# Optimization experiments

Measured on AMD Instinct MI355X. Metric: run time of the kernel, lower is better.

Reference implementation:

```python
import jax, jax.numpy as jnp
import numpy as np

NP_, NA_ = 50000, 20000
D_IN, D_HID, D_OUT = 128, 128, 64
E_W, E_C, E_R = 250000, 500000, 250000


def setup_inputs() -> dict:
    key = jax.random.key(0)
    ks = jax.random.split(key, 14)
    s_in = 1.0 / np.sqrt(D_IN)
    s_h = 1.0 / np.sqrt(D_HID)
    return {
        "x_paper": jax.random.normal(ks[0], (NP_, D_IN), jnp.float32),
        "x_author": jax.random.normal(ks[1], (NA_, D_IN), jnp.float32),
        "Wl1": jax.random.normal(ks[2], (3, D_HID, D_IN), jnp.float32) * s_in,
        "bl1": jax.random.normal(ks[3], (3, D_HID), jnp.float32) * 0.01,
        "Wr1": jax.random.normal(ks[4], (3, D_HID, D_IN), jnp.float32) * s_in,
        "Wl2": jax.random.normal(ks[5], (3, D_OUT, D_HID), jnp.float32) * s_h,
        "bl2": jax.random.normal(ks[6], (3, D_OUT), jnp.float32) * 0.01,
        "Wr2": jax.random.normal(ks[7], (3, D_OUT, D_HID), jnp.float32) * s_h,
        "writes_src": jax.random.randint(ks[8], (E_W,), 0, NA_),
        "writes_dst": jax.random.randint(ks[9], (E_W,), 0, NP_),
        "cites_src": jax.random.randint(ks[10], (E_C,), 0, NP_),
        "cites_dst": jax.random.randint(ks[11], (E_C,), 0, NP_),
        "rev_src": jax.random.randint(ks[12], (E_R,), 0, NP_),
        "rev_dst": jax.random.randint(ks[13], (E_R,), 0, NA_),
    }


def _sage(x_src, x_dst, src, dst, Wl, bl, Wr, n_dst):
    # PyG SAGEConv(aggr='mean'): lin_l(mean_j x_src[j]) + lin_r(x_dst)
    agg = jax.ops.segment_sum(x_src[src], dst, num_segments=n_dst)
    cnt = jax.ops.segment_sum(jnp.ones_like(dst, dtype=x_src.dtype), dst,
                              num_segments=n_dst)
    agg = agg / jnp.maximum(cnt, 1.0)[:, None]  # degree-0 nodes -> 0 (PyG scatter-mean)
    return agg @ Wl.T + bl + x_dst @ Wr.T


def reference(x_paper, x_author, Wl1, bl1, Wr1, Wl2, bl2, Wr2,
              writes_src, writes_dst, cites_src, cites_dst, rev_src, rev_dst):
    def hetero_layer(xp, xa, Wl, bl, Wr):
        # HeteroConv(aggr='mean'): average per-relation outputs per dst node type
        op = 0.5 * (_sage(xa, xp, writes_src, writes_dst, Wl[0], bl[0], Wr[0], NP_)
                    + _sage(xp, xp, cites_src, cites_dst, Wl[1], bl[1], Wr[1], NP_))
        oa = _sage(xp, xa, rev_src, rev_dst, Wl[2], bl[2], Wr[2], NA_)
        return op, oa

    hp, ha = hetero_layer(x_paper, x_author, Wl1, bl1, Wr1)
    hp, ha = jax.nn.relu(hp), jax.nn.relu(ha)  # norm_type='none', dropout eval-mode
    hp, _ = hetero_layer(hp, ha, Wl2, bl2, Wr2)
    return hp  # logits for category='paper', [NP_, D_OUT]
```

## Files before the change

### kernel.cpp

```cpp
#include <hip/hip_runtime.h>

#define NP 50000
#define NA 20000
#define E_W 250000
#define E_C 500000
#define E_R 250000
#define E_TOT (E_W + E_C + E_R)
#define CAP 48
#define RBLK 4096
#define NSEG 245
#define NCHP 782
#define NCHA 313
#define NBIN (NCHP + NCHA)

typedef __attribute__((ext_vector_type(8))) short short8;
typedef __attribute__((ext_vector_type(4))) float floatx4;
typedef __attribute__((ext_vector_type(2))) float floatx2;

__device__ __forceinline__ unsigned short f2bf(float f) {
    unsigned u = __float_as_uint(f);
    return (unsigned short)((u + 0x7FFFu + ((u >> 16) & 1u)) >> 16);
}
__device__ __forceinline__ float bflo(unsigned v) { return __uint_as_float(v << 16); }
__device__ __forceinline__ float bfhi(unsigned v) { return __uint_as_float(v & 0xFFFF0000u); }

__device__ __forceinline__ int frag_off(int NT, int j, int n, int k) {
    int t = n >> 4, ln = n & 15;
    int kb = k >> 5, q = (k >> 3) & 3, r = k & 7;
    return (((j * NT + t) * 4 + kb) * 64 + q * 16 + ln) * 8 + r;
}

__device__ __forceinline__ void prep_body(
    int idx,
    const float* __restrict__ xp, const float* __restrict__ xa,
    const float* __restrict__ Wl1, const float* __restrict__ Wr1,
    const float* __restrict__ Wl2, const float* __restrict__ Wr2,
    const float* __restrict__ bl1, const float* __restrict__ bl2,
    unsigned short* __restrict__ xpb, unsigned short* __restrict__ xab,
    unsigned* __restrict__ xp8, unsigned* __restrict__ xa8,
    unsigned short* __restrict__ Wp1, unsigned short* __restrict__ Wa1,
    unsigned short* __restrict__ Wt2, unsigned short* __restrict__ Wr2s,
    float* __restrict__ bias_p1, float* __restrict__ bias_a1,
    float* __restrict__ bias_p2) {
    const int n4p = NP * 32, n4a = NA * 32;
    if (idx < n4p + n4a) {
        const float* s; unsigned short* d; unsigned* d8; int i = idx;
        if (i < n4p) { s = xp; d = xpb; d8 = xp8; }
        else { s = xa; d = xab; d8 = xa8; i -= n4p; }
        float4 v = ((const float4*)s)[i];
        ushort4 u;
        u.x = f2bf(v.x); u.y = f2bf(v.y); u.z = f2bf(v.z); u.w = f2bf(v.w);
        ((ushort4*)d)[i] = u;
        int w = __builtin_amdgcn_cvt_pk_fp8_f32(v.x, v.y, 0, false);
        w = __builtin_amdgcn_cvt_pk_fp8_f32(v.z, v.w, w, true);
        d8[i] = (unsigned)w;
        return;
    }
    int j = idx - (n4p + n4a);
    if (j < 49152) {
        int jj = j >> 14, rem = j & 16383, n = rem >> 7, k = rem & 127;
        float v = (jj == 0)   ? 0.5f * Wl1[rem]
                  : (jj == 1) ? 0.5f * Wl1[16384 + rem]
                              : 0.5f * (Wr1[rem] + Wr1[16384 + rem]);
        Wp1[frag_off(8, jj, n, k)] = f2bf(v);
    } else if (j < 81920) {
        int i2 = j - 49152;
        int jj = i2 >> 14, rem = i2 & 16383, n = rem >> 7, k = rem & 127;
        float v = (jj == 0) ? Wl1[2 * 16384 + rem] : Wr1[2 * 16384 + rem];
        Wa1[frag_off(8, jj, n, k)] = f2bf(v);
    } else if (j < 98304) {
        int i2 = j - 81920;
        int jj = i2 >> 13, rem = i2 & 8191, n = rem >> 7, k = rem & 127;
        float v = 0.5f * Wl2[jj * 8192 + rem];
        Wt2[frag_off(4, jj, n, k)] = f2bf(v);
    } else if (j < 106496) {
        int i2 = j - 98304;
        int n = i2 >> 7, k = i2 & 127;
        float v = 0.5f * (Wr2[i2] + Wr2[8192 + i2]);
        Wr2s[frag_off(4, 0, n, k)] = f2bf(v);
    } else if (j < 106496 + 320) {
        int b = j - 106496;
        if (b < 128) bias_p1[b] = 0.5f * (bl1[b] + bl1[128 + b]);
        else if (b < 256) bias_a1[b - 128] = bl1[256 + b - 128];
        else bias_p2[b - 256] = 0.5f * (bl2[b - 256] + bl2[64 + b - 256]);
    }
}

__device__ __forceinline__ void edge_bin(
    int e, const int* __restrict__ w_src, const int* __restrict__ w_dst,
    const int* __restrict__ c_src, const int* __restrict__ c_dst,
    const int* __restrict__ r_src, const int* __restrict__ r_dst,
    int& bin, int& sub, int& src) {
    bool isC = (e >= E_W) & (e < E_W + E_C);
    bool isR = e >= E_W + E_C;
    const int* db = isR ? r_dst : (isC ? c_dst : w_dst);
    const int* sb = isR ? r_src : (isC ? c_src : w_src);
    int idx = e - (isC ? E_W : 0) - (isR ? (E_W + E_C) : 0);
    int d = db[idx];
    src = sb[idx];
    if (isR) { bin = NCHP + (d >> 6); sub = d & 63; }
    else { bin = d >> 6; sub = (d & 63) + (isC ? 64 : 0); }
}

__device__ __forceinline__ void route_body(
    int bid, const int* __restrict__ w_src, const int* __restrict__ w_dst,
    const int* __restrict__ c_src, const int* __restrict__ c_dst,
    const int* __restrict__ r_src, const int* __restrict__ r_dst,
    unsigned* __restrict__ seg, int* __restrict__ segoff, int* __restrict__ segcnt,
    int* cnt_s, int* base_s, int* cur_s) {
    int tid = threadIdx.x, lane = tid & 63;
    for (int k = tid; k < NBIN; k += 256) cnt_s[k] = 0;
    __syncthreads();
#pragma unroll 4
    for (int u = 0; u < 16; ++u) {
        int e = bid * RBLK + u * 256 + tid;
        if (e < E_TOT) {
            int bin, sub, src;
            edge_bin(e, w_src, w_dst, c_src, c_dst, r_src, r_dst, bin, sub, src);
            atomicAdd(&cnt_s[bin], 1);
        }
    }
    __syncthreads();
    if (tid < 64) {
        int v[18], tot = 0;
#pragma unroll
        for (int q = 0; q < 18; ++q) {
            int k = tid * 18 + q;
            v[q] = (k < NBIN) ? cnt_s[k] : 0;
            tot += v[q];
        }
        int sc = tot;
#pragma unroll
        for (int ofs = 1; ofs < 64; ofs <<= 1) {
            int t = __shfl_up(sc, ofs, 64);
            if (lane >= ofs) sc += t;
        }
        int run = sc - tot;
#pragma unroll
        for (int q = 0; q < 18; ++q) {
            int k = tid * 18 + q;
            if (k < NBIN) { base_s[k] = run; run += v[q]; }
        }
    }
    __syncthreads();
    for (int k = tid; k < NBIN; k += 256) {
        segoff[bid * NBIN + k] = base_s[k];
        segcnt[bid * NBIN + k] = cnt_s[k];
        cur_s[k] = base_s[k];
    }
    __syncthreads();
    unsigned* segb = seg + (size_t)bid * RBLK;
#pragma unroll 4
    for (int u = 0; u < 16; ++u) {
        int e = bid * RBLK + u * 256 + tid;
        if (e < E_TOT) {
            int bin, sub, src;
            edge_bin(e, w_src, w_dst, c_src, c_dst, r_src, r_dst, bin, sub, src);
            int pos = atomicAdd(&cur_s[bin], 1);
            segb[pos] = (unsigned)src | ((unsigned)sub << 16);
        }
    }
}

__global__ __launch_bounds__(256) void route_prep(
    const float* xp, const float* xa, const float* Wl1, const float* Wr1,
    const float* Wl2, const float* Wr2, const float* bl1, const float* bl2,
    unsigned short* xpb, unsigned short* xab, unsigned* xp8, unsigned* xa8,
    unsigned short* Wp1, unsigned short* Wa1, unsigned short* Wt2, unsigned short* Wr2s,
    float* bias_p1, float* bias_a1, float* bias_p2,
    const int* w_src, const int* w_dst, const int* c_src, const int* c_dst,
    const int* r_src, const int* r_dst,
    unsigned* seg, int* segoff, int* segcnt) {
    __shared__ int cnt_s[NBIN], base_s[NBIN], cur_s[NBIN];
    if ((int)blockIdx.x < NSEG)
        route_body(blockIdx.x, w_src, w_dst, c_src, c_dst, r_src, r_dst,
                   seg, segoff, segcnt, cnt_s, base_s, cur_s);
    else
        prep_body((blockIdx.x - NSEG) * 256 + threadIdx.x, xp, xa, Wl1, Wr1, Wl2, Wr2,
                  bl1, bl2, xpb, xab, xp8, xa8, Wp1, Wa1, Wt2, Wr2s,
                  bias_p1, bias_a1, bias_p2);
}

__global__ __launch_bounds__(512) void fill_l1(
    const unsigned* __restrict__ seg, const int* __restrict__ segoff,
    const int* __restrict__ segcnt, int* __restrict__ cnt,
    unsigned short* __restrict__ csr,
    const unsigned* __restrict__ xp8, const unsigned* __restrict__ xa8,
    const unsigned short* __restrict__ xpb, const unsigned short* __restrict__ xab,
    const unsigned short* __restrict__ Wp1, const float* __restrict__ bias_p1,
    const unsigned short* __restrict__ Wa1, const float* __restrict__ bias_a1,
    const unsigned short* __restrict__ Wt2, const unsigned short* __restrict__ Wr2s,
    unsigned short* __restrict__ ta, unsigned short* __restrict__ tp,
    float* __restrict__ sp) {
    __shared__ unsigned short rows[128 * CAP];
    __shared__ int cursor[128];
    __shared__ int offs[NSEG], cnts[NSEG];
    __shared__ __align__(16) unsigned short aggL[64][136];
    int tid = threadIdx.x;
    int k = blockIdx.x;
    bool isPaper = k < NCHP;
    int base = isPaper ? k * 64 : (k - NCHP) * 64;
    int total = isPaper ? NP : NA;
    int M = total - base; if (M > 64) M = 64;

    for (int s = tid; s < NSEG; s += 512) {
        offs[s] = segoff[s * NBIN + k];
        cnts[s] = segcnt[s * NBIN + k];
    }
    if (tid < 128) cursor[tid] = 0;
    __syncthreads();
    {
        int grp = tid >> 4, gl = tid & 15;
        for (int s = grp; s < NSEG; s += 32) {
            int n = cnts[s];
            const unsigned* spq = seg + (size_t)s * RBLK + offs[s];
            for (int i = gl; i < n; i += 16) {
                unsigned v = spq[i];
                int sub = v >> 16, srcn = v & 0xFFFFu;
                int pos = atomicAdd(&cursor[sub], 1);
                if (pos < CAP) rows[sub * CAP + pos] = (unsigned short)srcn;
            }
        }
    }
    __syncthreads();
    if (isPaper) {
        for (int r = tid; r < 2 * M; r += 512)
            cnt[base * 2 + r] = cursor[(r >> 1) + ((r & 1) << 6)];
        const unsigned* rU = (const unsigned*)rows;
        unsigned* cU = (unsigned*)csr + (size_t)base * 2 * (CAP / 2);
        for (int i = tid; i < 2 * M * (CAP / 2); i += 512) {
            int r = i / (CAP / 2), j = i - r * (CAP / 2);
            cU[i] = rU[((r >> 1) + ((r & 1) << 6)) * (CAP / 2) + j];
        }
    }

    int wave = tid >> 6, lane = tid & 63, ln = lane & 15, quad = lane >> 4;
    int wrow = (wave & 3) * 16, nhalf = wave >> 2;
    floatx4 acc[4];
#pragma unroll
    for (int t = 0; t < 4; ++t) acc[t] = (floatx4){0.f, 0.f, 0.f, 0.f};

    auto gather = [&](int rel, const unsigned* __restrict__ src8, int dummy) {
        int g = tid >> 5, sl = tid & 31;
        for (int l = g; l < 64; l += 16) {
            int deg = cursor[l + (rel << 6)];
            int degc = deg < CAP ? deg : CAP;
            const unsigned short* rp = &rows[(l + (rel << 6)) * CAP];
            float a0 = 0.f, a1 = 0.f, a2 = 0.f, a3 = 0.f;
            float b0 = 0.f, b1 = 0.f, b2 = 0.f, b3 = 0.f;
            for (int i = 0; i < degc; i += 8) {
                short8 rr = *(const short8*)&rp[i];
                unsigned v[8];
#pragma unroll
                for (int u = 0; u < 8; ++u) {
                    int ii = i + u;
                    int q = (ii < degc) ? (int)(unsigned short)rr[u] : dummy;
                    v[u] = src8[(q << 5) + sl];
                }
#pragma unroll
                for (int u = 0; u < 8; ++u) {
                    floatx2 lo = __builtin_amdgcn_cvt_pk_f32_fp8(v[u], false);
                    floatx2 hi = __builtin_amdgcn_cvt_pk_f32_fp8(v[u], true);
                    if (u & 1) { b0 += lo.x; b1 += lo.y; b2 += hi.x; b3 += hi.y; }
                    else       { a0 += lo.x; a1 += lo.y; a2 += hi.x; a3 += hi.y; }
                }
            }
            float scl = deg > 0 ? 1.f / (float)deg : 0.f;
            float r0 = (a0 + b0) * scl, r1 = (a1 + b1) * scl;
            float r2 = (a2 + b2) * scl, r3 = (a3 + b3) * scl;
            unsigned wlo = ((unsigned)f2bf(r1) << 16) | (unsigned)f2bf(r0);
            unsigned whi = ((unsigned)f2bf(r3) << 16) | (unsigned)f2bf(r2);
            *(uint2*)&aggL[l][sl * 4] = make_uint2(wlo, whi);
        }
    };
    auto gemm_lds = [&](const unsigned short* __restrict__ Wb) {
#pragma unroll
        for (int kb = 0; kb < 4; ++kb) {
            short8 af = *(const short8*)&aggL[wrow + ln][quad * 8 + kb * 32];
#pragma unroll
            for (int t = 0; t < 4; ++t) {
                short8 bf = *(const short8*)(Wb + ((nhalf * 4 + t) * 4 + kb) * 512 + lane * 8);
                acc[t] = __builtin_amdgcn_mfma_f32_16x16x32_bf16(af, bf, acc[t], 0, 0, 0);
            }
        }
    };
    auto gemm_glob = [&](const unsigned short* __restrict__ X,
                         const unsigned short* __restrict__ Wb) {
        int row = base + wrow + ln;
        int rowc = row < total ? row : total - 1;
        const unsigned short* A = X + (size_t)rowc * 128 + quad * 8;
#pragma unroll
        for (int kb = 0; kb < 4; ++kb) {
            short8 af = *(const short8*)(A + kb * 32);
#pragma unroll
            for (int t = 0; t < 4; ++t) {
                short8 bf = *(const short8*)(Wb + ((nhalf * 4 + t) * 4 + kb) * 512 + lane * 8);
                acc[t] = __builtin_amdgcn_mfma_f32_16x16x32_bf16(af, bf, acc[t], 0, 0, 0);
            }
        }
    };

    if (isPaper) {
        gather(0, xa8, NA);
        __syncthreads();
        gemm_lds(Wp1);
        __syncthreads();
        gather(1, xp8, NP);
        __syncthreads();
        gemm_lds(Wp1 + 16384);
        gemm_glob(xpb, Wp1 + 2 * 16384);
        __syncthreads();
    } else {
        gather(0, xp8, NP);
        __syncthreads();
        gemm_lds(Wa1);
        gemm_glob(xab, Wa1 + 16384);
        __syncthreads();
    }
    {
        const float* bias = isPaper ? bias_p1 : bias_a1;
#pragma unroll
        for (int t = 0; t < 4; ++t) {
            int col = nhalf * 64 + t * 16 + ln;
            float bv = bias[col];
#pragma unroll
            for (int r = 0; r < 4; ++r)
                aggL[wrow + quad * 4 + r][col] = f2bf(fmaxf(acc[t][r] + bv, 0.f));
        }
    }
    __syncthreads();
    floatx4 tacc[4];
#pragma unroll
    for (int t = 0; t < 4; ++t) tacc[t] = (floatx4){0.f, 0.f, 0.f, 0.f};
    int rows16 = (wave & 3) * 16;
    if (isPaper) {
        const unsigned short* W = (wave < 4) ? (Wt2 + 64 * 128) : Wr2s;
#pragma unroll
        for (int kb = 0; kb < 4; ++kb) {
            short8 af = *(const short8*)&aggL[rows16 + ln][quad * 8 + kb * 32];
#pragma unroll
            for (int t = 0; t < 4; ++t) {
                short8 bf = *(const short8*)(W + (t * 4 + kb) * 512 + lane * 8);
                tacc[t] = __builtin_amdgcn_mfma_f32_16x16x32_bf16(af, bf, tacc[t], 0, 0, 0);
            }
        }
#pragma unroll
        for (int t = 0; t < 4; ++t) {
            int col = t * 16 + ln;
#pragma unroll
            for (int r = 0; r < 4; ++r) {
                int lr = rows16 + quad * 4 + r;
                if (lr < M) {
                    if (wave < 4) tp[(size_t)(base + lr) * 64 + col] = f2bf(tacc[t][r]);
                    else sp[(size_t)(base + lr) * 64 + col] = tacc[t][r];
                }
            }
        }
    } else {
        int thalf = wave >> 2;
#pragma unroll
        for (int kb = 0; kb < 4; ++kb) {
            short8 af = *(const short8*)&aggL[rows16 + ln][quad * 8 + kb * 32];
#pragma unroll
            for (int tt = 0; tt < 2; ++tt) {
                short8 bf = *(const short8*)(Wt2 + ((thalf * 2 + tt) * 4 + kb) * 512 + lane * 8);
                tacc[tt] = __builtin_amdgcn_mfma_f32_16x16x32_bf16(af, bf, tacc[tt], 0, 0, 0);
            }
        }
#pragma unroll
        for (int tt = 0; tt < 2; ++tt) {
            int col = (thalf * 2 + tt) * 16 + ln;
#pragma unroll
            for (int r = 0; r < 4; ++r) {
                int lr = rows16 + quad * 4 + r;
                if (lr < M) ta[(size_t)(base + lr) * 64 + col] = f2bf(tacc[tt][r]);
            }
        }
    }
}

__global__ void agg2(const unsigned short* __restrict__ ta, const unsigned short* __restrict__ tp,
                     const int* __restrict__ cnt, const unsigned short* __restrict__ csr,
                     const float* __restrict__ sp_in, const float* __restrict__ bias_p2,
                     float* __restrict__ out) {
    int node = blockIdx.x * 8 + (threadIdx.x >> 5);
    if (node >= NP) return;
    int lane = threadIdx.x & 63;
    int sl = lane & 31;
    int hw = lane & 32;
    float r0 = 0.f, r1 = 0.f;
#pragma unroll
    for (int rel = 0; rel < 2; ++rel) {
        int dummy = (rel == 0) ? NA : NP;
        const unsigned* sp = (const unsigned*)((rel == 0) ? ta : tp);
        int idx = node * 2 + rel;
        int deg = cnt[idx];
        int degc = deg < CAP ? deg : CAP;
        const unsigned short* row = csr + (size_t)idx * CAP;
        int ei0 = (sl < degc) ? (int)row[sl] : dummy;
        int ei1 = (32 + sl < degc) ? (int)row[32 + sl] : dummy;
        int degw = degc;
        int other = __shfl_xor(degw, 32, 64);
        if (other > degw) degw = other;
        float s0 = 0.f, s1 = 0.f, t0 = 0.f, t1 = 0.f;
        for (int i = 0; i < degw; i += 8) {
            unsigned v[8];
#pragma unroll
            for (int u = 0; u < 8; ++u) {
                int ii = i + u;
                int esrc = (ii < 32) ? ei0 : ei1;
                int qq = __shfl(esrc, hw | (ii & 31), 64);
                qq = (ii < degc) ? qq : dummy;
                v[u] = sp[(qq << 5) + sl];
            }
#pragma unroll
            for (int u = 0; u < 8; ++u) {
                if (u & 1) { t0 += bflo(v[u]); t1 += bfhi(v[u]); }
                else       { s0 += bflo(v[u]); s1 += bfhi(v[u]); }
            }
        }
        float scl = deg > 0 ? 1.f / (float)deg : 0.f;
        r0 += (s0 + t0) * scl; r1 += (s1 + t1) * scl;
    }
    float2 spv = ((const float2*)sp_in)[(size_t)node * 32 + sl];
    float2 bv = ((const float2*)bias_p2)[sl];
    ((float2*)out)[(size_t)node * 32 + sl] =
        make_float2(r0 + spv.x + bv.x, r1 + spv.y + bv.y);
}

extern "C" void kernel_launch(void* const* d_in, const int* in_sizes, int n_in,
                              void* d_out, int out_size, void* d_ws, size_t ws_size,
                              hipStream_t stream) {
    (void)in_sizes; (void)n_in; (void)out_size; (void)ws_size;
    const float* xp  = (const float*)d_in[0];
    const float* xa  = (const float*)d_in[1];
    const float* Wl1 = (const float*)d_in[2];
    const float* bl1 = (const float*)d_in[3];
    const float* Wr1 = (const float*)d_in[4];
    const float* Wl2 = (const float*)d_in[5];
    const float* bl2 = (const float*)d_in[6];
    const float* Wr2 = (const float*)d_in[7];
    const int* w_src = (const int*)d_in[8];
    const int* w_dst = (const int*)d_in[9];
    const int* c_src = (const int*)d_in[10];
    const int* c_dst = (const int*)d_in[11];
    const int* r_src = (const int*)d_in[12];
    const int* r_dst = (const int*)d_in[13];
    float* out = (float*)d_out;

    char* p = (char*)d_ws;
    auto alloc = [&](size_t bytes) {
        char* r = p;
        p += (bytes + 255) & ~(size_t)255;
        return r;
    };
    unsigned short* xpb   = (unsigned short*)alloc((size_t)NP * 128 * 2);
    unsigned short* xab   = (unsigned short*)alloc((size_t)NA * 128 * 2);
    unsigned*       xp8   = (unsigned*)alloc((size_t)(NP + 1) * 128);
    unsigned*       xa8   = (unsigned*)alloc((size_t)(NA + 1) * 128);
    unsigned short* ta    = (unsigned short*)alloc((size_t)(NA + 1) * 64 * 2);
    unsigned short* tp    = (unsigned short*)alloc((size_t)(NP + 1) * 64 * 2);
    float*          sp    = (float*)alloc((size_t)NP * 64 * 4);
    int*            cnt    = (int*)alloc((size_t)NP * 2 * 4);
    unsigned short* csr    = (unsigned short*)alloc((size_t)NP * 2 * CAP * 2);
    unsigned*       seg    = (unsigned*)alloc((size_t)NSEG * RBLK * 4);
    int*            segoff = (int*)alloc((size_t)NSEG * NBIN * 4);
    int*            segcnt = (int*)alloc((size_t)NSEG * NBIN * 4);
    unsigned short* Wp1  = (unsigned short*)alloc(3 * 128 * 128 * 2);
    unsigned short* Wa1  = (unsigned short*)alloc(2 * 128 * 128 * 2);
    unsigned short* Wt2  = (unsigned short*)alloc(2 * 64 * 128 * 2);
    unsigned short* Wr2s = (unsigned short*)alloc(64 * 128 * 2);
    float* bias_p1 = (float*)alloc(128 * 4);
    float* bias_a1 = (float*)alloc(128 * 4);
    float* bias_p2 = (float*)alloc(64 * 4);

    hipMemsetAsync(xp8 + (size_t)NP * 32, 0, 128, stream);
    hipMemsetAsync(xa8 + (size_t)NA * 32, 0, 128, stream);
    hipMemsetAsync(ta + (size_t)NA * 64, 0, 128, stream);
    hipMemsetAsync(tp + (size_t)NP * 64, 0, 128, stream);

    int prep_threads = (NP + NA) * 32 + 106496 + 320;
    int prep_blocks = (prep_threads + 255) / 256;
    route_prep<<<NSEG + prep_blocks, 256, 0, stream>>>(
        xp, xa, Wl1, Wr1, Wl2, Wr2, bl1, bl2,
        xpb, xab, xp8, xa8, Wp1, Wa1, Wt2, Wr2s, bias_p1, bias_a1, bias_p2,
        w_src, w_dst, c_src, c_dst, r_src, r_dst, seg, segoff, segcnt);

    fill_l1<<<NBIN, 512, 0, stream>>>(seg, segoff, segcnt, cnt, csr,
                                      xp8, xa8, xpb, xab, Wp1, bias_p1, Wa1, bias_a1,
                                      Wt2, Wr2s, ta, tp, sp);

    agg2<<<(NP + 7) / 8, 256, 0, stream>>>(ta, tp, cnt, csr, sp, bias_p2, out);
}
```

Measured before the change: 199.1 us.

## Merge layer-1 relation gathers into one pass and halve routing segments

Routing blocks now cover 8192 edges each, halving the number of segments, and each segment's offset and count are packed into one 32-bit word. The layer-1 fused kernel gathers both relations (writes and cites) for all 128 local rows in a single pass, with each thread group processing two rows at once to get more loads in flight. The aggregation buffer is doubled to 128 rows so both GEMMs run back to back with fewer barriers, and the CSR write-out moves after the compute. The cost is more shared memory per block, which may reduce occupancy, and per-segment counts and offsets must stay below 65536.

```diff
diff --git a/kernel.cpp b/kernel.cpp
--- a/kernel.cpp
+++ b/kernel.cpp
@@ -7,8 +7,8 @@
 #define E_R 250000
 #define E_TOT (E_W + E_C + E_R)
 #define CAP 48
-#define RBLK 4096
-#define NSEG 245
+#define RBLK 8192
+#define NSEG 123
 #define NCHP 782
 #define NCHA 313
 #define NBIN (NCHP + NCHA)
@@ -106,13 +106,13 @@
     int bid, const int* __restrict__ w_src, const int* __restrict__ w_dst,
     const int* __restrict__ c_src, const int* __restrict__ c_dst,
     const int* __restrict__ r_src, const int* __restrict__ r_dst,
-    unsigned* __restrict__ seg, int* __restrict__ segoff, int* __restrict__ segcnt,
+    unsigned* __restrict__ seg, unsigned* __restrict__ segmeta,
     int* cnt_s, int* base_s, int* cur_s) {
     int tid = threadIdx.x, lane = tid & 63;
     for (int k = tid; k < NBIN; k += 256) cnt_s[k] = 0;
     __syncthreads();
 #pragma unroll 4
-    for (int u = 0; u < 16; ++u) {
+    for (int u = 0; u < 32; ++u) {
         int e = bid * RBLK + u * 256 + tid;
         if (e < E_TOT) {
             int bin, sub, src;
@@ -144,14 +144,13 @@
     }
     __syncthreads();
     for (int k = tid; k < NBIN; k += 256) {
-        segoff[bid * NBIN + k] = base_s[k];
-        segcnt[bid * NBIN + k] = cnt_s[k];
+        segmeta[bid * NBIN + k] = ((unsigned)base_s[k] << 16) | (unsigned)cnt_s[k];
         cur_s[k] = base_s[k];
     }
     __syncthreads();
     unsigned* segb = seg + (size_t)bid * RBLK;
 #pragma unroll 4
-    for (int u = 0; u < 16; ++u) {
+    for (int u = 0; u < 32; ++u) {
         int e = bid * RBLK + u * 256 + tid;
         if (e < E_TOT) {
             int bin, sub, src;
@@ -170,11 +169,11 @@
     float* bias_p1, float* bias_a1, float* bias_p2,
     const int* w_src, const int* w_dst, const int* c_src, const int* c_dst,
     const int* r_src, const int* r_dst,
-    unsigned* seg, int* segoff, int* segcnt) {
+    unsigned* seg, unsigned* segmeta) {
     __shared__ int cnt_s[NBIN], base_s[NBIN], cur_s[NBIN];
     if ((int)blockIdx.x < NSEG)
         route_body(blockIdx.x, w_src, w_dst, c_src, c_dst, r_src, r_dst,
-                   seg, segoff, segcnt, cnt_s, base_s, cur_s);
+                   seg, segmeta, cnt_s, base_s, cur_s);
     else
         prep_body((blockIdx.x - NSEG) * 256 + threadIdx.x, xp, xa, Wl1, Wr1, Wl2, Wr2,
                   bl1, bl2, xpb, xab, xp8, xa8, Wp1, Wa1, Wt2, Wr2s,
@@ -182,9 +181,8 @@
 }
 
 __global__ __launch_bounds__(512) void fill_l1(
-    const unsigned* __restrict__ seg, const int* __restrict__ segoff,
-    const int* __restrict__ segcnt, int* __restrict__ cnt,
-    unsigned short* __restrict__ csr,
+    const unsigned* __restrict__ seg, const unsigned* __restrict__ segmeta,
+    int* __restrict__ cnt, unsigned short* __restrict__ csr,
     const unsigned* __restrict__ xp8, const unsigned* __restrict__ xa8,
     const unsigned short* __restrict__ xpb, const unsigned short* __restrict__ xab,
     const unsigned short* __restrict__ Wp1, const float* __restrict__ bias_p1,
@@ -194,8 +192,8 @@
     float* __restrict__ sp) {
     __shared__ unsigned short rows[128 * CAP];
     __shared__ int cursor[128];
-    __shared__ int offs[NSEG], cnts[NSEG];
-    __shared__ __align__(16) unsigned short aggL[64][136];
+    __shared__ unsigned pkd[NSEG];
+    __shared__ __align__(16) unsigned short aggL[128][136];
     int tid = threadIdx.x;
     int k = blockIdx.x;
     bool isPaper = k < NCHP;
@@ -203,17 +201,15 @@
     int total = isPaper ? NP : NA;
     int M = total - base; if (M > 64) M = 64;
 
-    for (int s = tid; s < NSEG; s += 512) {
-        offs[s] = segoff[s * NBIN + k];
-        cnts[s] = segcnt[s * NBIN + k];
-    }
+    for (int s = tid; s < NSEG; s += 512) pkd[s] = segmeta[s * NBIN + k];
     if (tid < 128) cursor[tid] = 0;
     __syncthreads();
     {
         int grp = tid >> 4, gl = tid & 15;
         for (int s = grp; s < NSEG; s += 32) {
-            int n = cnts[s];
-            const unsigned* spq = seg + (size_t)s * RBLK + offs[s];
+            unsigned pk = pkd[s];
+            int n = pk & 0xFFFFu;
+            const unsigned* spq = seg + (size_t)s * RBLK + (pk >> 16);
             for (int i = gl; i < n; i += 16) {
                 unsigned v = spq[i];
                 int sub = v >> 16, srcn = v & 0xFFFFu;
@@ -223,6 +219,163 @@
         }
     }
     __syncthreads();
+    {
+        const unsigned* s0 = isPaper ? xa8 : xp8;
+        const unsigned* s1 = xp8;
+        int d0 = isPaper ? NA : NP, d1 = NP;
+        int LROWS = isPaper ? 128 : 64;
+        int g = tid >> 5, sl = tid & 31;
+        for (int l0 = g; l0 < LROWS; l0 += 32) {
+            int lA = l0, lB = l0 + 16;
+            const unsigned* sA = (lA & 64) ? s1 : s0;
+            const unsigned* sB = (lB & 64) ? s1 : s0;
+            int duA = (lA & 64) ? d1 : d0;
+            int duB = (lB & 64) ? d1 : d0;
+            int dA = cursor[lA], dB = cursor[lB];
+            int cA = dA < CAP ? dA : CAP, cB = dB < CAP ? dB : CAP;
+            int cm = cA > cB ? cA : cB;
+            const unsigned short* rpA = &rows[lA * CAP];
+            const unsigned short* rpB = &rows[lB * CAP];
+            float a0 = 0.f, a1 = 0.f, a2 = 0.f, a3 = 0.f;
+            float b0 = 0.f, b1 = 0.f, b2 = 0.f, b3 = 0.f;
+            for (int i = 0; i < cm; i += 8) {
+                short8 rA = *(const short8*)&rpA[i];
+                short8 rB = *(const short8*)&rpB[i];
+                unsigned vA[8], vB[8];
+#pragma unroll
+                for (int u = 0; u < 8; ++u) {
+                    int q = (i + u < cA) ? (int)(unsigned short)rA[u] : duA;
+                    vA[u] = sA[(q << 5) + sl];
+                }
+#pragma unroll
+                for (int u = 0; u < 8; ++u) {
+                    int q = (i + u < cB) ? (int)(unsigned short)rB[u] : duB;
+                    vB[u] = sB[(q << 5) + sl];
+                }
+#pragma unroll
+                for (int u = 0; u < 8; ++u) {
+                    floatx2 lo = __builtin_amdgcn_cvt_pk_f32_fp8(vA[u], false);
+                    floatx2 hi = __builtin_amdgcn_cvt_pk_f32_fp8(vA[u], true);
+                    a0 += lo.x; a1 += lo.y; a2 += hi.x; a3 += hi.y;
+                }
+#pragma unroll
+                for (int u = 0; u < 8; ++u) {
+                    floatx2 lo = __builtin_amdgcn_cvt_pk_f32_fp8(vB[u], false);
+                    floatx2 hi = __builtin_amdgcn_cvt_pk_f32_fp8(vB[u], true);
+                    b0 += lo.x; b1 += lo.y; b2 += hi.x; b3 += hi.y;
+                }
+            }
+            float sclA = dA > 0 ? 1.f / (float)dA : 0.f;
+            float sclB = dB > 0 ? 1.f / (float)dB : 0.f;
+            unsigned wloA = ((unsigned)f2bf(a1 * sclA) << 16) | (unsigned)f2bf(a0 * sclA);
+            unsigned whiA = ((unsigned)f2bf(a3 * sclA) << 16) | (unsigned)f2bf(a2 * sclA);
+            unsigned wloB = ((unsigned)f2bf(b1 * sclB) << 16) | (unsigned)f2bf(b0 * sclB);
+            unsigned whiB = ((unsigned)f2bf(b3 * sclB) << 16) | (unsigned)f2bf(b2 * sclB);
+            *(uint2*)&aggL[lA][sl * 4] = make_uint2(wloA, whiA);
+            *(uint2*)&aggL[lB][sl * 4] = make_uint2(wloB, whiB);
+        }
+    }
+    __syncthreads();
+    int wave = tid >> 6, lane = tid & 63, ln = lane & 15, quad = lane >> 4;
+    int wrow = (wave & 3) * 16, nhalf = wave >> 2;
+    floatx4 acc[4];
+#pragma unroll
+    for (int t = 0; t < 4; ++t) acc[t] = (floatx4){0.f, 0.f, 0.f, 0.f};
+    auto gemm_lds = [&](const unsigned short* __restrict__ Wb, int rowoff) {
+#pragma unroll
+        for (int kb = 0; kb < 4; ++kb) {
+            short8 af = *(const short8*)&aggL[rowoff + wrow + ln][quad * 8 + kb * 32];
+#pragma unroll
+            for (int t = 0; t < 4; ++t) {
+                short8 bf = *(const short8*)(Wb + ((nhalf * 4 + t) * 4 + kb) * 512 + lane * 8);
+                acc[t] = __builtin_amdgcn_mfma_f32_16x16x32_bf16(af, bf, acc[t], 0, 0, 0);
+            }
+        }
+    };
+    auto gemm_glob = [&](const unsigned short* __restrict__ X,
+                         const unsigned short* __restrict__ Wb) {
+        int row = base + wrow + ln;
+        int rowc = row < total ? row : total - 1;
+        const unsigned short* A = X + (size_t)rowc * 128 + quad * 8;
+#pragma unroll
+        for (int kb = 0; kb < 4; ++kb) {
+            short8 af = *(const short8*)(A + kb * 32);
+#pragma unroll
+            for (int t = 0; t < 4; ++t) {
+                short8 bf = *(const short8*)(Wb + ((nhalf * 4 + t) * 4 + kb) * 512 + lane * 8);
+                acc[t] = __builtin_amdgcn_mfma_f32_16x16x32_bf16(af, bf, acc[t], 0, 0, 0);
+            }
+        }
+    };
+    if (isPaper) {
+        gemm_lds(Wp1, 0);
+        gemm_lds(Wp1 + 16384, 64);
+        gemm_glob(xpb, Wp1 + 2 * 16384);
+    } else {
+        gemm_lds(Wa1, 0);
+        gemm_glob(xab, Wa1 + 16384);
+    }
+    __syncthreads();
+    {
+        const float* bias = isPaper ? bias_p1 : bias_a1;
+#pragma unroll
+        for (int t = 0; t < 4; ++t) {
+            int col = nhalf * 64 + t * 16 + ln;
+            float bv = bias[col];
+#pragma unroll
+            for (int r = 0; r < 4; ++r)
+                aggL[wrow + quad * 4 + r][col] = f2bf(fmaxf(acc[t][r] + bv, 0.f));
+        }
+    }
+    __syncthreads();
+    floatx4 tacc[4];
+#pragma unroll
+    for (int t = 0; t < 4; ++t) tacc[t] = (floatx4){0.f, 0.f, 0.f, 0.f};
+    int rows16 = (wave & 3) * 16;
+    if (isPaper) {
+        const unsigned short* W = (wave < 4) ? (Wt2 + 64 * 128) : Wr2s;
+#pragma unroll
+        for (int kb = 0; kb < 4; ++kb) {
+            short8 af = *(const short8*)&aggL[rows16 + ln][quad * 8 + kb * 32];
+#pragma unroll
+            for (int t = 0; t < 4; ++t) {
+                short8 bf = *(const short8*)(W + (t * 4 + kb) * 512 + lane * 8);
+                tacc[t] = __builtin_amdgcn_mfma_f32_16x16x32_bf16(af, bf, tacc[t], 0, 0, 0);
+            }
+        }
+#pragma unroll
+        for (int t = 0; t < 4; ++t) {
+            int col = t * 16 + ln;
+#pragma unroll
+            for (int r = 0; r < 4; ++r) {
+                int lr = rows16 + quad * 4 + r;
+                if (lr < M) {
+                    if (wave < 4) tp[(size_t)(base + lr) * 64 + col] = f2bf(tacc[t][r]);
+                    else sp[(size_t)(base + lr) * 64 + col] = tacc[t][r];
+                }
+            }
+        }
+    } else {
+        int thalf = wave >> 2;
+#pragma unroll
+        for (int kb = 0; kb < 4; ++kb) {
+            short8 af = *(const short8*)&aggL[rows16 + ln][quad * 8 + kb * 32];
+#pragma unroll
+            for (int tt = 0; tt < 2; ++tt) {
+                short8 bf = *(const short8*)(Wt2 + ((thalf * 2 + tt) * 4 + kb) * 512 + lane * 8);
+                tacc[tt] = __builtin_amdgcn_mfma_f32_16x16x32_bf16(af, bf, tacc[tt], 0, 0, 0);
+            }
+        }
+#pragma unroll
+        for (int tt = 0; tt < 2; ++tt) {
+            int col = (thalf * 2 + tt) * 16 + ln;
+#pragma unroll
+            for (int r = 0; r < 4; ++r) {
+                int lr = rows16 + quad * 4 + r;
+                if (lr < M) ta[(size_t)(base + lr) * 64 + col] = f2bf(tacc[tt][r]);
+            }
+        }
+    }
     if (isPaper) {
         for (int r = tid; r < 2 * M; r += 512)
             cnt[base * 2 + r] = cursor[(r >> 1) + ((r & 1) << 6)];
@@ -231,150 +384,6 @@
         for (int i = tid; i < 2 * M * (CAP / 2); i += 512) {
             int r = i / (CAP / 2), j = i - r * (CAP / 2);
             cU[i] = rU[((r >> 1) + ((r & 1) << 6)) * (CAP / 2) + j];
-        }
-    }
-
-    int wave = tid >> 6, lane = tid & 63, ln = lane & 15, quad = lane >> 4;
-    int wrow = (wave & 3) * 16, nhalf = wave >> 2;
-    floatx4 acc[4];
-#pragma unroll
-    for (int t = 0; t < 4; ++t) acc[t] = (floatx4){0.f, 0.f, 0.f, 0.f};
-
-    auto gather = [&](int rel, const unsigned* __restrict__ src8, int dummy) {
-        int g = tid >> 5, sl = tid & 31;
-        for (int l = g; l < 64; l += 16) {
-            int deg = cursor[l + (rel << 6)];
-            int degc = deg < CAP ? deg : CAP;
-            const unsigned short* rp = &rows[(l + (rel << 6)) * CAP];
-            float a0 = 0.f, a1 = 0.f, a2 = 0.f, a3 = 0.f;
-            float b0 = 0.f, b1 = 0.f, b2 = 0.f, b3 = 0.f;
-            for (int i = 0; i < degc; i += 8) {
-                short8 rr = *(const short8*)&rp[i];
-                unsigned v[8];
-#pragma unroll
-                for (int u = 0; u < 8; ++u) {
-                    int ii = i + u;
-                    int q = (ii < degc) ? (int)(unsigned short)rr[u] : dummy;
-                    v[u] = src8[(q << 5) + sl];
-                }
-#pragma unroll
-                for (int u = 0; u < 8; ++u) {
-                    floatx2 lo = __builtin_amdgcn_cvt_pk_f32_fp8(v[u], false);
-                    floatx2 hi = __builtin_amdgcn_cvt_pk_f32_fp8(v[u], true);
-                    if (u & 1) { b0 += lo.x; b1 += lo.y; b2 += hi.x; b3 += hi.y; }
-                    else       { a0 += lo.x; a1 += lo.y; a2 += hi.x; a3 += hi.y; }
-                }
-            }
-            float scl = deg > 0 ? 1.f / (float)deg : 0.f;
-            float r0 = (a0 + b0) * scl, r1 = (a1 + b1) * scl;
-            float r2 = (a2 + b2) * scl, r3 = (a3 + b3) * scl;
-            unsigned wlo = ((unsigned)f2bf(r1) << 16) | (unsigned)f2bf(r0);
-            unsigned whi = ((unsigned)f2bf(r3) << 16) | (unsigned)f2bf(r2);
-            *(uint2*)&aggL[l][sl * 4] = make_uint2(wlo, whi);
-        }
-    };
-    auto gemm_lds = [&](const unsigned short* __restrict__ Wb) {
-#pragma unroll
-        for (int kb = 0; kb < 4; ++kb) {
-            short8 af = *(const short8*)&aggL[wrow + ln][quad * 8 + kb * 32];
-#pragma unroll
-            for (int t = 0; t < 4; ++t) {
-                short8 bf = *(const short8*)(Wb + ((nhalf * 4 + t) * 4 + kb) * 512 + lane * 8);
-                acc[t] = __builtin_amdgcn_mfma_f32_16x16x32_bf16(af, bf, acc[t], 0, 0, 0);
-            }
-        }
-    };
-    auto gemm_glob = [&](const unsigned short* __restrict__ X,
-                         const unsigned short* __restrict__ Wb) {
-        int row = base + wrow + ln;
-        int rowc = row < total ? row : total - 1;
-        const unsigned short* A = X + (size_t)rowc * 128 + quad * 8;
-#pragma unroll
-        for (int kb = 0; kb < 4; ++kb) {
-            short8 af = *(const short8*)(A + kb * 32);
-#pragma unroll
-            for (int t = 0; t < 4; ++t) {
-                short8 bf = *(const short8*)(Wb + ((nhalf * 4 + t) * 4 + kb) * 512 + lane * 8);
-                acc[t] = __builtin_amdgcn_mfma_f32_16x16x32_bf16(af, bf, acc[t], 0, 0, 0);
-            }
-        }
-    };
-
-    if (isPaper) {
-        gather(0, xa8, NA);
-        __syncthreads();
-        gemm_lds(Wp1);
-        __syncthreads();
-        gather(1, xp8, NP);
-        __syncthreads();
-        gemm_lds(Wp1 + 16384);
-        gemm_glob(xpb, Wp1 + 2 * 16384);
-        __syncthreads();
-    } else {
-        gather(0, xp8, NP);
-        __syncthreads();
-        gemm_lds(Wa1);
-        gemm_glob(xab, Wa1 + 16384);
-        __syncthreads();
-    }
-    {
-        const float* bias = isPaper ? bias_p1 : bias_a1;
-#pragma unroll
-        for (int t = 0; t < 4; ++t) {
-            int col = nhalf * 64 + t * 16 + ln;
-            float bv = bias[col];
-#pragma unroll
-            for (int r = 0; r < 4; ++r)
-                aggL[wrow + quad * 4 + r][col] = f2bf(fmaxf(acc[t][r] + bv, 0.f));
-        }
-    }
-    __syncthreads();
-    floatx4 tacc[4];
-#pragma unroll
-    for (int t = 0; t < 4; ++t) tacc[t] = (floatx4){0.f, 0.f, 0.f, 0.f};
-    int rows16 = (wave & 3) * 16;
-    if (isPaper) {
-        const unsigned short* W = (wave < 4) ? (Wt2 + 64 * 128) : Wr2s;
-#pragma unroll
-        for (int kb = 0; kb < 4; ++kb) {
-            short8 af = *(const short8*)&aggL[rows16 + ln][quad * 8 + kb * 32];
-#pragma unroll
-            for (int t = 0; t < 4; ++t) {
-                short8 bf = *(const short8*)(W + (t * 4 + kb) * 512 + lane * 8);
-                tacc[t] = __builtin_amdgcn_mfma_f32_16x16x32_bf16(af, bf, tacc[t], 0, 0, 0);
-            }
-        }
-#pragma unroll
-        for (int t = 0; t < 4; ++t) {
-            int col = t * 16 + ln;
-#pragma unroll
-            for (int r = 0; r < 4; ++r) {
-                int lr = rows16 + quad * 4 + r;
-                if (lr < M) {
-                    if (wave < 4) tp[(size_t)(base + lr) * 64 + col] = f2bf(tacc[t][r]);
-                    else sp[(size_t)(base + lr) * 64 + col] = tacc[t][r];
-                }
-            }
-        }
-    } else {
-        int thalf = wave >> 2;
-#pragma unroll
-        for (int kb = 0; kb < 4; ++kb) {
-            short8 af = *(const short8*)&aggL[rows16 + ln][quad * 8 + kb * 32];
-#pragma unroll
-            for (int tt = 0; tt < 2; ++tt) {
-                short8 bf = *(const short8*)(Wt2 + ((thalf * 2 + tt) * 4 + kb) * 512 + lane * 8);
-                tacc[tt] = __builtin_amdgcn_mfma_f32_16x16x32_bf16(af, bf, tacc[tt], 0, 0, 0);
-            }
-        }
-#pragma unroll
-        for (int tt = 0; tt < 2; ++tt) {
-            int col = (thalf * 2 + tt) * 16 + ln;
-#pragma unroll
-            for (int r = 0; r < 4; ++r) {
-                int lr = rows16 + quad * 4 + r;
-                if (lr < M) ta[(size_t)(base + lr) * 64 + col] = f2bf(tacc[tt][r]);
-            }
         }
     }
 }
@@ -461,11 +470,10 @@
     unsigned short* ta    = (unsigned short*)alloc((size_t)(NA + 1) * 64 * 2);
     unsigned short* tp    = (unsigned short*)alloc((size_t)(NP + 1) * 64 * 2);
     float*          sp    = (float*)alloc((size_t)NP * 64 * 4);
-    int*            cnt    = (int*)alloc((size_t)NP * 2 * 4);
-    unsigned short* csr    = (unsigned short*)alloc((size_t)NP * 2 * CAP * 2);
-    unsigned*       seg    = (unsigned*)alloc((size_t)NSEG * RBLK * 4);
-    int*            segoff = (int*)alloc((size_t)NSEG * NBIN * 4);
-    int*            segcnt = (int*)alloc((size_t)NSEG * NBIN * 4);
+    int*            cnt     = (int*)alloc((size_t)NP * 2 * 4);
+    unsigned short* csr     = (unsigned short*)alloc((size_t)NP * 2 * CAP * 2);
+    unsigned*       seg     = (unsigned*)alloc((size_t)NSEG * RBLK * 4);
+    unsigned*       segmeta = (unsigned*)alloc((size_t)NSEG * NBIN * 4);
     unsigned short* Wp1  = (unsigned short*)alloc(3 * 128 * 128 * 2);
     unsigned short* Wa1  = (unsigned short*)alloc(2 * 128 * 128 * 2);
     unsigned short* Wt2  = (unsigned short*)alloc(2 * 64 * 128 * 2);
@@ -484,9 +492,9 @@
     route_prep<<<NSEG + prep_blocks, 256, 0, stream>>>(
         xp, xa, Wl1, Wr1, Wl2, Wr2, bl1, bl2,
         xpb, xab, xp8, xa8, Wp1, Wa1, Wt2, Wr2s, bias_p1, bias_a1, bias_p2,
-        w_src, w_dst, c_src, c_dst, r_src, r_dst, seg, segoff, segcnt);
-
-    fill_l1<<<NBIN, 512, 0, stream>>>(seg, segoff, segcnt, cnt, csr,
+        w_src, w_dst, c_src, c_dst, r_src, r_dst, seg, segmeta);
+
+    fill_l1<<<NBIN, 512, 0, stream>>>(seg, segmeta, cnt, csr,
                                       xp8, xa8, xpb, xab, Wp1, bias_p1, Wa1, bias_a1,
                                       Wt2, Wr2s, ta, tp, sp);
 
```

New measurement: 204.0 us. 2.4% more time.
